# Performance work log

Measured on AMD Instinct MI355X. Metric: run time of the kernel, lower is better.

## Reference

```python
import jax, jax.numpy as jnp
import numpy as np

N = 10000        # nodes
E = 160000       # edges (before self loops)
F_IN = 4         # n_features
D = 128          # d_model (per-head out channels for GAT, GCN width)
H = 8            # n_heads
NEG_SLOPE = 0.2  # PyG GATConv default leaky relu slope


def setup_inputs() -> dict:
    key = jax.random.key(0)
    ks = jax.random.split(key, 10)
    x = jax.random.normal(ks[0], (N, F_IN), dtype=jnp.float32)
    edge_index = jax.random.randint(ks[1], (2, E), 0, N, dtype=jnp.int64)
    s = 0.05
    gat_w = jax.random.normal(ks[2], (F_IN, H * D), dtype=jnp.float32) * s
    att_src = jax.random.normal(ks[3], (H, D), dtype=jnp.float32) * s
    att_dst = jax.random.normal(ks[4], (H, D), dtype=jnp.float32) * s
    gat_b = jnp.zeros((H * D,), dtype=jnp.float32)
    gcn1_w = jax.random.normal(ks[5], (H * D, D), dtype=jnp.float32) * s
    gcn1_b = jnp.zeros((D,), dtype=jnp.float32)
    gcn2_w = jax.random.normal(ks[6], (D, D), dtype=jnp.float32) * s
    gcn2_b = jnp.zeros((D,), dtype=jnp.float32)
    return {"x": x, "edge_index": edge_index, "gat_w": gat_w,
            "att_src": att_src, "att_dst": att_dst, "gat_b": gat_b,
            "gcn1_w": gcn1_w, "gcn1_b": gcn1_b,
            "gcn2_w": gcn2_w, "gcn2_b": gcn2_b}


def _add_self_loops(edge_index, n):
    loops = jnp.arange(n, dtype=edge_index.dtype)
    src = jnp.concatenate([edge_index[0], loops])
    dst = jnp.concatenate([edge_index[1], loops])
    return src, dst


def _gat_conv(x, src, dst, w, att_src, att_dst, b):
    # PyG GATConv, concat=True: h [N,H,D]
    h = (x @ w).reshape(-1, H, D)
    a_s = jnp.einsum('nhd,hd->nh', h, att_src)   # per-node src score
    a_d = jnp.einsum('nhd,hd->nh', h, att_dst)   # per-node dst score
    e = jax.nn.leaky_relu(a_s[src] + a_d[dst], NEG_SLOPE)  # [Etot,H]
    # segment softmax over destination node, per head
    m = jax.ops.segment_max(e, dst, num_segments=N)
    ex = jnp.exp(e - m[dst])
    denom = jax.ops.segment_sum(ex, dst, num_segments=N)
    alpha = ex / denom[dst]                       # [Etot,H]
    msg = h[src] * alpha[:, :, None]              # [Etot,H,D]
    out = jax.ops.segment_sum(msg, dst, num_segments=N)  # [N,H,D]
    return out.reshape(-1, H * D) + b


def _gcn_conv(x, src, dst, w, b):
    # PyG GCNConv with symmetric normalization (self loops already added)
    h = x @ w
    deg = jax.ops.segment_sum(jnp.ones_like(dst, dtype=h.dtype), dst,
                              num_segments=N)
    dinv = jnp.where(deg > 0, jax.lax.rsqrt(deg), 0.0)
    norm = dinv[src] * dinv[dst]                  # [Etot]
    out = jax.ops.segment_sum(h[src] * norm[:, None], dst, num_segments=N)
    return out + b


def reference(x, edge_index, gat_w, att_src, att_dst, gat_b,
              gcn1_w, gcn1_b, gcn2_w, gcn2_b):
    src, dst = _add_self_loops(edge_index, N)
    h = _gat_conv(x, src, dst, gat_w, att_src, att_dst, gat_b)
    h = jax.nn.gelu(h, approximate=False)         # torch F.gelu is exact erf
    h = _gcn_conv(h, src, dst, gcn1_w, gcn1_b)
    h = jax.nn.gelu(h, approximate=False)
    h = _gcn_conv(h, src, dst, gcn2_w, gcn2_b)
    return h                                      # [N, D]
```

## Files before the change

### kernel.cpp

```cpp
#include <hip/hip_runtime.h>
#include <math.h>

#define HEADS 8
#define DHEAD 128
#define CMODEL 1024
#define BCAP 64

typedef __attribute__((ext_vector_type(8))) short bf16x8;
typedef __attribute__((ext_vector_type(4))) float f32x4;

__device__ __forceinline__ float gelu_exact(float x) {
    return 0.5f * x * (1.0f + erff(x * 0.70710678118654752440f));
}

__device__ __forceinline__ unsigned short f2bf(float f) {
    unsigned u = __float_as_uint(f);
    return (unsigned short)((u + 0x7FFFu + ((u >> 16) & 1u)) >> 16);
}
__device__ __forceinline__ float bf2f(unsigned short h) {
    return __uint_as_float((unsigned)h << 16);
}

__global__ void __launch_bounds__(256) k_scores(const float* __restrict__ x,
                                                const float* __restrict__ gat_w,
                                                const float* __restrict__ att_src,
                                                const float* __restrict__ att_dst,
                                                const float* __restrict__ W1,
                                                const float* __restrict__ W2,
                                                float* __restrict__ xpack,
                                                float* __restrict__ a_d,
                                                int* __restrict__ cursor,
                                                int* __restrict__ bucket,
                                                unsigned short* __restrict__ W1hi,
                                                unsigned short* __restrict__ W1lo,
                                                unsigned short* __restrict__ W2hi,
                                                unsigned short* __restrict__ W2lo,
                                                int n_nodes, int nb_scores) {
    {
        int gidz = blockIdx.x * 256 + threadIdx.x;
        int total = gridDim.x * 256;
        int nvec = n_nodes * 16;
        for (int i = gidz; i < nvec; i += total)
            ((int4*)bucket)[i] = make_int4(0, 0, 0, 0);
    }
    if ((int)blockIdx.x >= nb_scores) {
        int t = (blockIdx.x - nb_scores) * 256 + threadIdx.x;
        const int total1 = (1024 >> 5) * 8 * 64;
        const int total2 = (128 >> 5) * 8 * 64;
        const float* W; unsigned short *Whi, *Wlo;
        if (t < total1) { W = W1; Whi = W1hi; Wlo = W1lo; }
        else if (t < total1 + total2) { t -= total1; W = W2; Whi = W2hi; Wlo = W2lo; }
        else return;
        int lane = t & 63;
        int ct = (t >> 6) & 7;
        int kc = t >> 9;
        int quad = lane >> 4;
        int col = ct * 16 + (lane & 15);
        size_t o = (size_t)t * 8;
        #pragma unroll
        for (int j = 0; j < 8; j++) {
            float w = W[(size_t)(kc * 32 + quad * 8 + j) * 128 + col];
            unsigned short h = f2bf(w);
            Whi[o + j] = h;
            Wlo[o + j] = f2bf(w - bf2f(h));
        }
        return;
    }
    __shared__ float ws_s[32], ws_d[32];
    int t = threadIdx.x;
    if (t < 64) {
        int e = t >> 1;
        int which = t & 1;
        int hh = e >> 2, k = e & 3;
        const float* wrow = gat_w + k * CMODEL + hh * DHEAD;
        const float* av = which ? (att_dst + hh * DHEAD) : (att_src + hh * DHEAD);
        float s = 0.0f;
        for (int c = 0; c < DHEAD; c++) s += wrow[c] * av[c];
        if (which) ws_d[e] = s; else ws_s[e] = s;
    }
    int gid = blockIdx.x * 256 + t;
    if (gid < n_nodes) cursor[gid] = 0;
    __syncthreads();
    int p = gid;
    if (p >= n_nodes * HEADS) return;
    int n = p >> 3, hh = p & 7;
    float4 xv = *(const float4*)(x + (size_t)n * 4);
    float4 ws = *(const float4*)&ws_s[hh * 4];
    float4 wd = *(const float4*)&ws_d[hh * 4];
    a_d[p] = xv.x * wd.x + xv.y * wd.y + xv.z * wd.z + xv.w * wd.w;
    xpack[(size_t)n * 16 + 4 + hh] =
        xv.x * ws.x + xv.y * ws.y + xv.z * ws.z + xv.w * ws.w;
    if (hh == 0) *(float4*)(xpack + (size_t)n * 16) = xv;
}

__global__ void __launch_bounds__(256) k_scatter(const int* __restrict__ ei,
                                                 int* __restrict__ cursor,
                                                 int* __restrict__ bucket,
                                                 int n_nodes, int n_edges) {
    int e = blockIdx.x * 256 + threadIdx.x;
    int etot = n_edges + n_nodes;
    if (e >= etot) return;
    int s, d;
    if (e < n_edges) { s = ei[e]; d = ei[n_edges + e]; }
    else             { s = d = e - n_edges; }
    int pos = atomicAdd(&cursor[d], 1);
    if (pos < BCAP) bucket[(d << 6) + pos] = s;
}

__global__ void __launch_bounds__(256, 3) k_smax_mm1(const float* __restrict__ xpack,
                                                  const float* __restrict__ a_d,
                                                  const int* __restrict__ deg,
                                                  const int* __restrict__ bucket,
                                                  const float* __restrict__ gat_w,
                                                  const float* __restrict__ gat_b,
                                                  const unsigned short* __restrict__ Bhi,
                                                  const unsigned short* __restrict__ Blo,
                                                  float* __restrict__ t,
                                                  int n_nodes) {
    __shared__ float xs[16 * 32];
    __shared__ float ck[2][16 * 68];
    int mb = blockIdx.x;
    int tid = threadIdx.x;
    int lane = tid & 63;
    int w = tid >> 6;

    bf16x8 bhA[2][2], blA[2][2], bhB[2][2], blB[2][2];
    #pragma unroll
    for (int kc2 = 0; kc2 < 2; kc2++)
        #pragma unroll
        for (int ct = 0; ct < 2; ct++) {
            size_t bi = (((size_t)(kc2 * 8) + w * 2 + ct) * 64 + lane) * 8;
            bhA[kc2][ct] = *(const bf16x8*)(Bhi + bi);
            blA[kc2][ct] = *(const bf16x8*)(Blo + bi);
        }

    {
        int q = tid >> 1;
        int half = tid & 1;
        int ln = tid >> 4, hh = q & 7;
        int n = mb * 16 + ln;
        int nc = (n < n_nodes) ? n : (n_nodes - 1);
        int grp = lane & 48;
        int gl = lane & 15;
        int basec = nc << 6;
        int pre0 = bucket[basec + gl];
        int pre1 = bucket[basec + 16 + gl];
        int pre2 = bucket[basec + 32 + gl];
        int pre3 = bucket[basec + 48 + gl];
        auto SRC = [&](int e) -> int {
            int v = (e < 16) ? pre0 : (e < 32) ? pre1 : (e < 48) ? pre2 : pre3;
            return __shfl(v, grp + (e & 15), 64);
        };
        float sum = 0.0f;
        float4 acc = make_float4(0, 0, 0, 0);
        if (n < n_nodes) {
            int dg = deg[n]; if (dg > BCAP) dg = BCAP;
            float ad = a_d[n * 8 + hh];
            int nbat = (dg + 15) >> 4;
            for (int b = 0; b < nbat; b++) {
                int rbase = b * 16 + half;
                int ss[8]; float4 xv[8]; float es[8];
                #pragma unroll
                for (int i = 0; i < 8; i++) ss[i] = SRC(rbase + 2 * i);
                #pragma unroll
                for (int i = 0; i < 8; i++) {
                    const float* ps = xpack + (size_t)ss[i] * 16;
                    xv[i] = *(const float4*)ps;
                    es[i] = ps[4 + hh];
                }
                #pragma unroll
                for (int i = 0; i < 8; i++) {
                    float e = es[i] + ad;
                    e = (e > 0.0f) ? e : 0.2f * e;
                    float wg = (rbase + 2 * i < dg) ? __expf(e) : 0.0f;
                    sum += wg;
                    acc.x += wg * xv[i].x;
                    acc.y += wg * xv[i].y;
                    acc.z += wg * xv[i].z;
                    acc.w += wg * xv[i].w;
                }
            }
        }
        sum   += __shfl_down(sum, 1);
        acc.x += __shfl_down(acc.x, 1);
        acc.y += __shfl_down(acc.y, 1);
        acc.z += __shfl_down(acc.z, 1);
        acc.w += __shfl_down(acc.w, 1);
        if (half == 0) {
            float inv = (sum > 0.0f) ? (1.0f / sum) : 0.0f;
            *(float4*)&xs[q * 4] = make_float4(acc.x * inv, acc.y * inv,
                                               acc.z * inv, acc.w * inv);
        }
    }
    __syncthreads();

    int lm = lane & 15, quad = lane >> 4;
    int cc = tid & 63;
    int rp = tid >> 6;
    f32x4 macc[2];
    macc[0] = (f32x4){0.0f, 0.0f, 0.0f, 0.0f};
    macc[1] = (f32x4){0.0f, 0.0f, 0.0f, 0.0f};

#define ROUND(RR, BH, BL, BH_N, BL_N, RNEXT)                                    \
    {                                                                           \
        int buf = (RR) & 1;                                                     \
        int col = (RR) * 64 + cc;                                               \
        float w0 = gat_w[col], w1 = gat_w[1024 + col],                          \
              w2 = gat_w[2048 + col], w3 = gat_w[3072 + col];                   \
        float bb = gat_b[col];                                                  \
        int hh2 = (RR) >> 1;                                                    \
        _Pragma("unroll")                                                       \
        for (int rr = 0; rr < 4; rr++) {                                        \
            int row = rp * 4 + rr;                                              \
            float4 xa = *(const float4*)&xs[(row * 8 + hh2) * 4];               \
            float v = xa.x * w0 + xa.y * w1 + xa.z * w2 + xa.w * w3 + bb;       \
            ck[buf][row * 68 + cc] = gelu_exact(v);                             \
        }                                                                       \
        _Pragma("unroll")                                                       \
        for (int kc2 = 0; kc2 < 2; kc2++)                                       \
            _Pragma("unroll")                                                   \
            for (int ct = 0; ct < 2; ct++) {                                    \
                size_t bi = (((size_t)((RNEXT) * 2 + kc2) * 8 + w * 2 + ct) * 64 + lane) * 8; \
                BH_N[kc2][ct] = *(const bf16x8*)(Bhi + bi);                     \
                BL_N[kc2][ct] = *(const bf16x8*)(Blo + bi);                     \
            }                                                                   \
        asm volatile("s_waitcnt lgkmcnt(0)" ::: "memory");                      \
        __builtin_amdgcn_s_barrier();                                           \
        __builtin_amdgcn_sched_barrier(0);                                      \
        _Pragma("unroll")                                                       \
        for (int kc2 = 0; kc2 < 2; kc2++) {                                     \
            float a[8];                                                         \
            *(float4*)&a[0] = *(const float4*)&ck[buf][lm * 68 + kc2 * 32 + quad * 8];     \
            *(float4*)&a[4] = *(const float4*)&ck[buf][lm * 68 + kc2 * 32 + quad * 8 + 4]; \
            bf16x8 ah, al;                                                      \
            _Pragma("unroll")                                                   \
            for (int j = 0; j < 8; j++) {                                       \
                unsigned short h = f2bf(a[j]);                                  \
                ah[j] = (short)h;                                               \
                al[j] = (short)f2bf(a[j] - bf2f(h));                            \
            }                                                                   \
            _Pragma("unroll")                                                   \
            for (int ct = 0; ct < 2; ct++) {                                    \
                macc[ct] = __builtin_amdgcn_mfma_f32_16x16x32_bf16(ah, BH[kc2][ct], macc[ct], 0, 0, 0); \
                macc[ct] = __builtin_amdgcn_mfma_f32_16x16x32_bf16(al, BH[kc2][ct], macc[ct], 0, 0, 0); \
                macc[ct] = __builtin_amdgcn_mfma_f32_16x16x32_bf16(ah, BL[kc2][ct], macc[ct], 0, 0, 0); \
            }                                                                   \
        }                                                                       \
    }

    for (int r = 0; r < 16; r += 2) {
        ROUND(r,     bhA, blA, bhB, blB, r + 1);
        ROUND(r + 1, bhB, blB, bhA, blA, (r + 2 < 16 ? r + 2 : 15));
    }
#undef ROUND

    #pragma unroll
    for (int ct = 0; ct < 2; ct++) {
        int col = (w * 2 + ct) * 16 + lm;
        #pragma unroll
        for (int reg = 0; reg < 4; reg++) {
            int row = mb * 16 + quad * 4 + reg;
            if (row < n_nodes) {
                float dv = 1.0f / sqrtf((float)deg[row]);
                t[(size_t)row * 128 + col] = macc[ct][reg] * dv;
            }
        }
    }
}

__global__ void __launch_bounds__(512) k_gcn1_fused(const float* __restrict__ t,
                                                    const int* __restrict__ deg,
                                                    const int* __restrict__ bucket,
                                                    const float* __restrict__ bias,
                                                    const unsigned short* __restrict__ Bhi,
                                                    const unsigned short* __restrict__ Blo,
                                                    float* __restrict__ t2,
                                                    int n_nodes) {
    __shared__ float hs[16][132];
    int tid = threadIdx.x;
    int mb = blockIdx.x;
    int c = tid & 31;
    int ln = tid >> 5;
    int node = mb * 16 + ln;
    int nc = (node < n_nodes) ? node : (n_nodes - 1);
    int base = nc << 6;
    int sa = bucket[base + c];
    int sb = bucket[base + 32 + c];
    int dgt = (node < n_nodes) ? deg[node] : 1;
    int dg = dgt > BCAP ? BCAP : dgt;
    float dn = 1.0f / sqrtf((float)dgt);
    int d1 = dg > 32 ? 32 : dg;
    #pragma unroll
    for (int h2 = 0; h2 < 2; h2++) {
        const float* tp = t + h2 * 64 + c * 2;
        float2 acc = make_float2(0.0f, 0.0f);
        int r = 0;
        for (; r + 4 <= d1; r += 4) {
            int s0 = __shfl(sa, r + 0, 32);
            int s1 = __shfl(sa, r + 1, 32);
            int s2 = __shfl(sa, r + 2, 32);
            int s3 = __shfl(sa, r + 3, 32);
            float2 v0 = *(const float2*)(tp + (size_t)s0 * 128);
            float2 v1 = *(const float2*)(tp + (size_t)s1 * 128);
            float2 v2 = *(const float2*)(tp + (size_t)s2 * 128);
            float2 v3 = *(const float2*)(tp + (size_t)s3 * 128);
            acc.x += v0.x + v1.x + v2.x + v3.x;
            acc.y += v0.y + v1.y + v2.y + v3.y;
        }
        for (; r < d1; r++) {
            int s = __shfl(sa, r, 32);
            float2 v = *(const float2*)(tp + (size_t)s * 128);
            acc.x += v.x; acc.y += v.y;
        }
        for (; r < dg; r++) {
            int s = __shfl(sb, r - 32, 32);
            float2 v = *(const float2*)(tp + (size_t)s * 128);
            acc.x += v.x; acc.y += v.y;
        }
        int k = h2 * 64 + c * 2;
        float2 bb = *(const float2*)(bias + k);
        hs[ln][k]     = gelu_exact(acc.x * dn + bb.x);
        hs[ln][k + 1] = gelu_exact(acc.y * dn + bb.y);
    }
    __syncthreads();
    int lane = tid & 63;
    int w = tid >> 6;
    int lm = lane & 15, quad = lane >> 4;
    f32x4 acc2 = (f32x4){0.0f, 0.0f, 0.0f, 0.0f};
    #pragma unroll
    for (int kc = 0; kc < 4; kc++) {
        float a[8];
        *(float4*)&a[0] = *(const float4*)&hs[lm][kc * 32 + quad * 8];
        *(float4*)&a[4] = *(const float4*)&hs[lm][kc * 32 + quad * 8 + 4];
        bf16x8 ah, al;
        #pragma unroll
        for (int j = 0; j < 8; j++) {
            unsigned short h = f2bf(a[j]);
            ah[j] = (short)h;
            al[j] = (short)f2bf(a[j] - bf2f(h));
        }
        bf16x8 bh = *(const bf16x8*)(Bhi + (((size_t)(kc * 8 + w)) * 64 + lane) * 8);
        bf16x8 bl = *(const bf16x8*)(Blo + (((size_t)(kc * 8 + w)) * 64 + lane) * 8);
        acc2 = __builtin_amdgcn_mfma_f32_16x16x32_bf16(ah, bh, acc2, 0, 0, 0);
        acc2 = __builtin_amdgcn_mfma_f32_16x16x32_bf16(al, bh, acc2, 0, 0, 0);
        acc2 = __builtin_amdgcn_mfma_f32_16x16x32_bf16(ah, bl, acc2, 0, 0, 0);
    }
    int col = w * 16 + lm;
    #pragma unroll
    for (int reg = 0; reg < 4; reg++) {
        int row = mb * 16 + quad * 4 + reg;
        if (row < n_nodes) {
            float dv = 1.0f / sqrtf((float)deg[row]);
            t2[(size_t)row * 128 + col] = acc2[reg] * dv;
        }
    }
}

__global__ void __launch_bounds__(256) k_gcn_agg(const float* __restrict__ t,
                                                 const int* __restrict__ deg,
                                                 const int* __restrict__ bucket,
                                                 const float* __restrict__ bias,
                                                 float* __restrict__ outF,
                                                 int n_nodes) {
    int c = threadIdx.x & 31;
    int ln = threadIdx.x >> 5;
    int n = blockIdx.x * 8 + ln;
    int col0 = blockIdx.y * 64;
    if (n >= n_nodes) return;
    float2 acc = make_float2(0.0f, 0.0f);
    int dgt = deg[n];
    int dg = dgt > BCAP ? BCAP : dgt;
    int base = n << 6;
    int sa = bucket[base + c];
    int sb = bucket[base + 32 + c];
    const float* tp = t + col0 + c * 2;
    int d1 = dg > 32 ? 32 : dg;
    int r = 0;
    for (; r + 4 <= d1; r += 4) {
        int s0 = __shfl(sa, r + 0, 32);
        int s1 = __shfl(sa, r + 1, 32);
        int s2 = __shfl(sa, r + 2, 32);
        int s3 = __shfl(sa, r + 3, 32);
        float2 v0 = *(const float2*)(tp + (size_t)s0 * 128);
        float2 v1 = *(const float2*)(tp + (size_t)s1 * 128);
        float2 v2 = *(const float2*)(tp + (size_t)s2 * 128);
        float2 v3 = *(const float2*)(tp + (size_t)s3 * 128);
        acc.x += v0.x + v1.x + v2.x + v3.x;
        acc.y += v0.y + v1.y + v2.y + v3.y;
    }
    for (; r < d1; r++) {
        int s = __shfl(sa, r, 32);
        float2 v = *(const float2*)(tp + (size_t)s * 128);
        acc.x += v.x; acc.y += v.y;
    }
    for (; r < dg; r++) {
        int s = __shfl(sb, r - 32, 32);
        float2 v = *(const float2*)(tp + (size_t)s * 128);
        acc.x += v.x; acc.y += v.y;
    }
    float dn = 1.0f / sqrtf((float)dgt);
    int k = col0 + c * 2;
    float2 bb = *(const float2*)(bias + k);
    *(float2*)(outF + (size_t)n * 128 + k) =
        make_float2(acc.x * dn + bb.x, acc.y * dn + bb.y);
}

extern "C" void kernel_launch(void* const* d_in, const int* in_sizes, int n_in,
                              void* d_out, int out_size, void* d_ws, size_t ws_size,
                              hipStream_t stream) {
    const float* x        = (const float*)d_in[0];
    const int*   ei       = (const int*)d_in[1];
    const float* gat_w    = (const float*)d_in[2];
    const float* att_src  = (const float*)d_in[3];
    const float* att_dst  = (const float*)d_in[4];
    const float* gat_b    = (const float*)d_in[5];
    const float* gcn1_w   = (const float*)d_in[6];
    const float* gcn1_b   = (const float*)d_in[7];
    const float* gcn2_w   = (const float*)d_in[8];
    const float* gcn2_b   = (const float*)d_in[9];
    float* out = (float*)d_out;

    int N = in_sizes[0] / 4;
    int E = in_sizes[1] / 2;
    int Etot = E + N;
    int n_mtiles = (N + 15) / 16;

    char* base = (char*)d_ws;
    float*          t      = (float*)(base);
    float*          t2     = (float*)(base + 5120000);
    unsigned short* w1hi   = (unsigned short*)(base + 26000000);
    unsigned short* w1lo   = (unsigned short*)(base + 26262144);
    unsigned short* w2hi   = (unsigned short*)(base + 26524288);
    unsigned short* w2lo   = (unsigned short*)(base + 26557056);
    size_t off = 81920000;
    float* xpack  = (float*)(base + off); off += (size_t)N * 16 * 4;
    float* a_d    = (float*)(base + off); off += (size_t)N * 8 * 4;
    int*   cursor = (int*)(base + off);   off += (size_t)N * 4;
    int*   bucket = (int*)(base + off);   off += (size_t)N * BCAP * 4;

    int nb_scores = (N * HEADS + 255) / 256;
    int nb_wswz   = (16384 + 2048 + 255) / 256;

    k_scores<<<nb_scores + nb_wswz, 256, 0, stream>>>(x, gat_w, att_src, att_dst,
                                                      gcn1_w, gcn2_w, xpack, a_d, cursor,
                                                      bucket, w1hi, w1lo, w2hi, w2lo,
                                                      N, nb_scores);

    k_scatter<<<(Etot + 255) / 256, 256, 0, stream>>>(ei, cursor, bucket, N, E);

    k_smax_mm1<<<n_mtiles, 256, 0, stream>>>(xpack, a_d, cursor, bucket,
                                             gat_w, gat_b, w1hi, w1lo, t, N);

    k_gcn1_fused<<<n_mtiles, 512, 0, stream>>>(t, cursor, bucket, gcn1_b,
                                               w2hi, w2lo, t2, N);

    k_gcn_agg<<<dim3((N + 7) / 8, 2), 256, 0, stream>>>(t2, cursor, bucket, gcn2_b,
                                                        out, N);
}
```

Measured before the change: 152.8 us.

## Halve node tile in fused GAT softmax+GEMM kernel to double block count

The fused GAT aggregation plus first GCN GEMM kernel now processes 8 nodes per block instead of 16. Each node gets 32 threads, 4 per head, instead of 16 threads, 2 per head, with an extra shuffle reduction step. The MFMA tile's upper 8 rows are zero-padded in shared memory and the grid doubles, with launch bounds raised to 4 blocks per CU. The aim is more parallelism and occupancy for 10000 nodes. The cost is that half of the MFMA work is wasted on padding and the B-weight loads are repeated across twice as many blocks.

```diff
diff --git a/kernel.cpp b/kernel.cpp
--- a/kernel.cpp
+++ b/kernel.cpp
@@ -107,7 +107,7 @@
     if (pos < BCAP) bucket[(d << 6) + pos] = s;
 }
 
-__global__ void __launch_bounds__(256, 3) k_smax_mm1(const float* __restrict__ xpack,
+__global__ void __launch_bounds__(256, 4) k_smax_mm1(const float* __restrict__ xpack,
                                                   const float* __restrict__ a_d,
                                                   const int* __restrict__ deg,
                                                   const int* __restrict__ bucket,
@@ -117,12 +117,19 @@
                                                   const unsigned short* __restrict__ Blo,
                                                   float* __restrict__ t,
                                                   int n_nodes) {
-    __shared__ float xs[16 * 32];
+    __shared__ float xs[8 * 32];
     __shared__ float ck[2][16 * 68];
     int mb = blockIdx.x;
     int tid = threadIdx.x;
     int lane = tid & 63;
     int w = tid >> 6;
+
+    {
+        int zr = 8 + (tid >> 6);
+        int zc = tid & 63;
+        ck[0][zr * 68 + zc] = 0.0f; ck[0][(zr + 4) * 68 + zc] = 0.0f;
+        ck[1][zr * 68 + zc] = 0.0f; ck[1][(zr + 4) * 68 + zc] = 0.0f;
+    }
 
     bf16x8 bhA[2][2], blA[2][2], bhB[2][2], blB[2][2];
     #pragma unroll
@@ -135,33 +142,31 @@
         }
 
     {
-        int q = tid >> 1;
-        int half = tid & 1;
-        int ln = tid >> 4, hh = q & 7;
-        int n = mb * 16 + ln;
+        int ln = tid >> 5;
+        int g = tid & 31;
+        int hh = g >> 2;
+        int quarter = g & 3;
+        int n = mb * 8 + ln;
         int nc = (n < n_nodes) ? n : (n_nodes - 1);
-        int grp = lane & 48;
-        int gl = lane & 15;
         int basec = nc << 6;
-        int pre0 = bucket[basec + gl];
-        int pre1 = bucket[basec + 16 + gl];
-        int pre2 = bucket[basec + 32 + gl];
-        int pre3 = bucket[basec + 48 + gl];
+        int sa = bucket[basec + g];
+        int sb = bucket[basec + 32 + g];
+        int grp = lane & 32;
         auto SRC = [&](int e) -> int {
-            int v = (e < 16) ? pre0 : (e < 32) ? pre1 : (e < 48) ? pre2 : pre3;
-            return __shfl(v, grp + (e & 15), 64);
+            int v = (e < 32) ? sa : sb;
+            return __shfl(v, grp + (e & 31), 64);
         };
         float sum = 0.0f;
         float4 acc = make_float4(0, 0, 0, 0);
         if (n < n_nodes) {
             int dg = deg[n]; if (dg > BCAP) dg = BCAP;
             float ad = a_d[n * 8 + hh];
-            int nbat = (dg + 15) >> 4;
+            int nbat = (dg > 32) ? 2 : 1;
             for (int b = 0; b < nbat; b++) {
-                int rbase = b * 16 + half;
+                int rbase = b * 32 + quarter;
                 int ss[8]; float4 xv[8]; float es[8];
                 #pragma unroll
-                for (int i = 0; i < 8; i++) ss[i] = SRC(rbase + 2 * i);
+                for (int i = 0; i < 8; i++) ss[i] = SRC(rbase + 4 * i);
                 #pragma unroll
                 for (int i = 0; i < 8; i++) {
                     const float* ps = xpack + (size_t)ss[i] * 16;
@@ -172,7 +177,7 @@
                 for (int i = 0; i < 8; i++) {
                     float e = es[i] + ad;
                     e = (e > 0.0f) ? e : 0.2f * e;
-                    float wg = (rbase + 2 * i < dg) ? __expf(e) : 0.0f;
+                    float wg = (rbase + 4 * i < dg) ? __expf(e) : 0.0f;
                     sum += wg;
                     acc.x += wg * xv[i].x;
                     acc.y += wg * xv[i].y;
@@ -186,10 +191,15 @@
         acc.y += __shfl_down(acc.y, 1);
         acc.z += __shfl_down(acc.z, 1);
         acc.w += __shfl_down(acc.w, 1);
-        if (half == 0) {
+        sum   += __shfl_down(sum, 2);
+        acc.x += __shfl_down(acc.x, 2);
+        acc.y += __shfl_down(acc.y, 2);
+        acc.z += __shfl_down(acc.z, 2);
+        acc.w += __shfl_down(acc.w, 2);
+        if (quarter == 0) {
             float inv = (sum > 0.0f) ? (1.0f / sum) : 0.0f;
-            *(float4*)&xs[q * 4] = make_float4(acc.x * inv, acc.y * inv,
-                                               acc.z * inv, acc.w * inv);
+            *(float4*)&xs[(ln * 8 + hh) * 4] = make_float4(acc.x * inv, acc.y * inv,
+                                                           acc.z * inv, acc.w * inv);
         }
     }
     __syncthreads();
@@ -210,8 +220,8 @@
         float bb = gat_b[col];                                                  \
         int hh2 = (RR) >> 1;                                                    \
         _Pragma("unroll")                                                       \
-        for (int rr = 0; rr < 4; rr++) {                                        \
-            int row = rp * 4 + rr;                                              \
+        for (int rr = 0; rr < 2; rr++) {                                        \
+            int row = rp * 2 + rr;                                              \
             float4 xa = *(const float4*)&xs[(row * 8 + hh2) * 4];               \
             float v = xa.x * w0 + xa.y * w1 + xa.z * w2 + xa.w * w3 + bb;       \
             ck[buf][row * 68 + cc] = gelu_exact(v);                             \
@@ -259,8 +269,9 @@
         int col = (w * 2 + ct) * 16 + lm;
         #pragma unroll
         for (int reg = 0; reg < 4; reg++) {
-            int row = mb * 16 + quad * 4 + reg;
-            if (row < n_nodes) {
+            int rr = quad * 4 + reg;
+            int row = mb * 8 + rr;
+            if (rr < 8 && row < n_nodes) {
                 float dv = 1.0f / sqrtf((float)deg[row]);
                 t[(size_t)row * 128 + col] = macc[ct][reg] * dv;
             }
@@ -448,8 +459,8 @@
 
     k_scatter<<<(Etot + 255) / 256, 256, 0, stream>>>(ei, cursor, bucket, N, E);
 
-    k_smax_mm1<<<n_mtiles, 256, 0, stream>>>(xpack, a_d, cursor, bucket,
-                                             gat_w, gat_b, w1hi, w1lo, t, N);
+    k_smax_mm1<<<(N + 7) / 8, 256, 0, stream>>>(xpack, a_d, cursor, bucket,
+                                                gat_w, gat_b, w1hi, w1lo, t, N);
 
     k_gcn1_fused<<<n_mtiles, 512, 0, stream>>>(t, cursor, bucket, gcn1_b,
                                                w2hi, w2lo, t2, N);
```

Result: slower. 176.7 us (+15.7%).
